# Optimization experiments

Measured on AMD Instinct MI355X. Metric: run time of the kernel, lower is better.

## Reference

```python
import jax, jax.numpy as jnp
import numpy as np
import math


def _bandwidth(d):
    # gz = 2*Gamma((d+1)/2)/Gamma(d/2); use lgamma for numerical stability.
    gz = 2.0 * math.exp(math.lgamma(0.5 * (d + 1)) - math.lgamma(0.5 * d))
    return 1.0 / (2.0 * gz * gz)


def _kernel_mean(xa, xb, gamma):
    # mean over the [Na, Nb] RBF kernel matrix, squared distance via matmul identity
    sq = (jnp.sum(xa * xa, axis=1)[:, None]
          + jnp.sum(xb * xb, axis=1)[None, :]
          - 2.0 * (xa @ xb.T))
    sq = jnp.maximum(sq, 0.0)  # guard tiny negatives from the identity
    return jnp.mean(jnp.exp(-gamma * sq))


def setup_inputs() -> dict:
    key = jax.random.key(0)
    k1, k2 = jax.random.split(key)
    x1 = jax.random.normal(k1, (8192, 128), dtype=jnp.float32)
    x2 = jax.random.normal(k2, (8192, 128), dtype=jnp.float32)
    return {"x1": x1, "x2": x2}


def reference(x1, x2):
    g1 = _bandwidth(x1.shape[1])
    g2 = _bandwidth(x2.shape[1])
    m11 = _kernel_mean(x1, x1, g1)
    m22 = _kernel_mean(x2, x2, g2)
    m12 = _kernel_mean(x1, x2, g1)
    return jnp.sqrt(m11 - 2.0 * m12 + m22)
```

## Files before the change

### kernel.cpp

```cpp
#include <hip/hip_runtime.h>
#include <cmath>

#define D 128
#define BM 128
#define BK 64
#define LOG2E 1.4426950408889634

typedef __attribute__((ext_vector_type(8))) _Float16 f16x8;
typedef __attribute__((ext_vector_type(4))) float f32x4;
typedef __attribute__((ext_vector_type(2))) float f32x2;

__device__ __forceinline__ void async_cp16(const void* g, void* l) {
    __builtin_amdgcn_global_load_lds(
        (__attribute__((address_space(1))) void*)g,
        (__attribute__((address_space(3))) void*)l, 16, 0, 0);
}

__global__ __launch_bounds__(256) void prep_kernel(
    const float* __restrict__ x1, const float* __restrict__ x2,
    _Float16* __restrict__ xh, float* __restrict__ El,
    double* __restrict__ acc, float gl, int N) {
    int tid = threadIdx.x;
    if (blockIdx.x == 0 && tid < 64) acc[tid] = 0.0;
    int r = blockIdx.x * 16 + (tid >> 4);
    if (r >= 2 * N) return;
    int l = tid & 15;
    const float* row = (r < N) ? x1 + (size_t)r * D : x2 + (size_t)(r - N) * D;
    float4 v0 = ((const float4*)row)[l * 2];
    float4 v1 = ((const float4*)row)[l * 2 + 1];
    float v[8] = {v0.x, v0.y, v0.z, v0.w, v1.x, v1.y, v1.z, v1.w};
    float p = 0.f;
    _Float16 h8[8];
#pragma unroll
    for (int j = 0; j < 8; ++j) {
        p = fmaf(v[j], v[j], p);
        h8[j] = (_Float16)v[j];
    }
    *(uint4*)(xh + (size_t)r * D + l * 8) = *(uint4*)h8;
#pragma unroll
    for (int off = 8; off; off >>= 1) p += __shfl_down(p, off, 16);
    if (l == 0) El[r] = gl * p;
}

__global__ __launch_bounds__(256, 4) void mmd_mfma_kernel(
    const _Float16* __restrict__ xh, const float* __restrict__ El,
    double* __restrict__ acc, float c2l, int N) {
    __shared__ float4 smem[2048];

    int t = blockIdx.x;
    int bi = (int)((sqrtf(8.0f * t + 1.0f) - 1.0f) * 0.5f);
    while ((bi + 1) * (bi + 2) / 2 <= t) ++bi;
    while (bi * (bi + 1) / 2 > t) --bi;
    int bj = t - bi * (bi + 1) / 2;

    int half = N / BM;
    float w = (bi == bj) ? 1.0f : 2.0f;
    if ((bi < half) != (bj < half)) w = -2.0f;
    int aBase = bi * BM, bBase = bj * BM;

    int tid = threadIdx.x;
    int lane = tid & 63, wave = tid >> 6;
    int quad = lane >> 4, l16 = lane & 15;
    int wrow = (wave & 1) * 64, wcol = (wave >> 1) * 64;

    const _Float16* gsrc[8];
    float4* ldst[8];
#pragma unroll
    for (int r = 0; r < 2; ++r) {
        int rowBase = r ? bBase : aBase;
#pragma unroll
        for (int i = 0; i < 4; ++i) {
            int slot = i * 256 + tid;
            int row = slot >> 3;
            int kc4 = (slot & 7) ^ (row & 7);
            gsrc[r * 4 + i] = xh + ((size_t)(rowBase + row) * D + kc4 * 8);
            ldst[r * 4 + i] = &smem[r * 1024 + slot];
        }
    }

    f32x4 C[4][4];
#pragma unroll
    for (int i = 0; i < 4; ++i)
#pragma unroll
        for (int j = 0; j < 4; ++j) C[i][j] = {0.f, 0.f, 0.f, 0.f};

    for (int c = 0; c < 2; ++c) {
        if (c) __syncthreads();
        int koff = c * BK;
#pragma unroll
        for (int q = 0; q < 8; ++q) async_cp16(gsrc[q] + koff, ldst[q]);
        __syncthreads();
#pragma unroll
        for (int s = 0; s < 2; ++s) {
            int kc4 = s * 4 + quad;
            f16x8 a[4], b[4];
#pragma unroll
            for (int u = 0; u < 4; ++u) {
                int ar = wrow + u * 16 + l16;
                a[u] = *(const f16x8*)&smem[ar * 8 + (kc4 ^ (ar & 7))];
                int br = wcol + u * 16 + l16;
                b[u] = *(const f16x8*)&smem[1024 + br * 8 + (kc4 ^ (br & 7))];
            }
#pragma unroll
            for (int ti = 0; ti < 4; ++ti)
#pragma unroll
                for (int tj = 0; tj < 4; ++tj)
                    C[ti][tj] = __builtin_amdgcn_mfma_f32_16x16x32_f16(
                        a[ti], b[tj], C[ti][tj], 0, 0, 0);
        }
    }

    int arow0 = aBase + wrow + quad * 4;
    int bcol0 = bBase + wcol + l16;
    float4 ea4[4];
#pragma unroll
    for (int ti = 0; ti < 4; ++ti) ea4[ti] = *(const float4*)&El[arow0 + ti * 16];
    f32x2 cc = {c2l, c2l};
    float lsum = 0.f;
#pragma unroll
    for (int tj = 0; tj < 4; ++tj) {
        float eb = El[bcol0 + tj * 16];
        f32x2 p = {0.f, 0.f};
#pragma unroll
        for (int ti = 0; ti < 4; ++ti) {
            f32x4 d = C[ti][tj];
            f32x2 a01 = cc * f32x2{d.x, d.y} + f32x2{ea4[ti].x, ea4[ti].y};
            f32x2 a23 = cc * f32x2{d.z, d.w} + f32x2{ea4[ti].z, ea4[ti].w};
            f32x2 e, e2;
            e.x = __builtin_amdgcn_exp2f(a01.x);
            e.y = __builtin_amdgcn_exp2f(a01.y);
            e2.x = __builtin_amdgcn_exp2f(a23.x);
            e2.y = __builtin_amdgcn_exp2f(a23.y);
            p += e + e2;
        }
        lsum = fmaf(p.x + p.y, __builtin_amdgcn_exp2f(eb), lsum);
    }
    double ds = (double)lsum * (double)w;
#pragma unroll
    for (int off = 32; off; off >>= 1) ds += __shfl_down(ds, off);
    __syncthreads();
    double* red = (double*)smem;
    if (lane == 0) red[wave] = ds;
    __syncthreads();
    if (tid == 0)
        atomicAdd(&acc[(bi + bj) & 63], red[0] + red[1] + red[2] + red[3]);
}

__global__ __launch_bounds__(64) void mmd_finalize_kernel(
    const double* __restrict__ acc, float* __restrict__ out, int N) {
    int l = threadIdx.x;
    double v = acc[l];
#pragma unroll
    for (int off = 32; off; off >>= 1) v += __shfl_down(v, off);
    if (l == 0) {
        double nn = (double)N * (double)N;
        double s = v / nn;
        out[0] = (float)sqrt(s > 0.0 ? s : 0.0);
    }
}

extern "C" void kernel_launch(void* const* d_in, const int* in_sizes, int n_in,
                              void* d_out, int out_size, void* d_ws, size_t ws_size,
                              hipStream_t stream) {
    const float* x1 = (const float*)d_in[0];
    const float* x2 = (const float*)d_in[1];
    int N = in_sizes[0] / D;

    double* acc = (double*)d_ws;
    float* El = (float*)((char*)d_ws + 8192);
    _Float16* xh = (_Float16*)((char*)d_ws + 73728);

    double lg = lgamma(0.5 * (D + 1)) - lgamma(0.5 * D);
    double gz = 2.0 * exp(lg);
    double gamma = 1.0 / (2.0 * gz * gz);
    float gl = (float)(-gamma * LOG2E);
    float c2l = (float)(2.0 * gamma * LOG2E);

    prep_kernel<<<(2 * N + 15) / 16, 256, 0, stream>>>(x1, x2, xh, El, acc, gl, N);

    int nt2 = 2 * N / BM;
    int nblocks = nt2 * (nt2 + 1) / 2;
    mmd_mfma_kernel<<<nblocks, 256, 0, stream>>>(xh, El, acc, c2l, N);

    mmd_finalize_kernel<<<1, 64, 0, stream>>>(acc, (float*)d_out, N);
}
```

Measured before the change: 109.4 us.

## Load MFMA operands directly from global memory instead of staging through LDS

```diff
diff --git a/kernel.cpp b/kernel.cpp
--- a/kernel.cpp
+++ b/kernel.cpp
@@ -3,18 +3,11 @@
 
 #define D 128
 #define BM 128
-#define BK 64
 #define LOG2E 1.4426950408889634
 
 typedef __attribute__((ext_vector_type(8))) _Float16 f16x8;
 typedef __attribute__((ext_vector_type(4))) float f32x4;
 typedef __attribute__((ext_vector_type(2))) float f32x2;
-
-__device__ __forceinline__ void async_cp16(const void* g, void* l) {
-    __builtin_amdgcn_global_load_lds(
-        (__attribute__((address_space(1))) void*)g,
-        (__attribute__((address_space(3))) void*)l, 16, 0, 0);
-}
 
 __global__ __launch_bounds__(256) void prep_kernel(
     const float* __restrict__ x1, const float* __restrict__ x2,
@@ -45,7 +38,7 @@
 __global__ __launch_bounds__(256, 4) void mmd_mfma_kernel(
     const _Float16* __restrict__ xh, const float* __restrict__ El,
     double* __restrict__ acc, float c2l, int N) {
-    __shared__ float4 smem[2048];
+    __shared__ double red[4];
 
     int t = blockIdx.x;
     int bi = (int)((sqrtf(8.0f * t + 1.0f) - 1.0f) * 0.5f);
@@ -63,19 +56,12 @@
     int quad = lane >> 4, l16 = lane & 15;
     int wrow = (wave & 1) * 64, wcol = (wave >> 1) * 64;
 
-    const _Float16* gsrc[8];
-    float4* ldst[8];
+    const char* xb = (const char*)xh;
+    unsigned offA[4], offB[4];
 #pragma unroll
-    for (int r = 0; r < 2; ++r) {
-        int rowBase = r ? bBase : aBase;
-#pragma unroll
-        for (int i = 0; i < 4; ++i) {
-            int slot = i * 256 + tid;
-            int row = slot >> 3;
-            int kc4 = (slot & 7) ^ (row & 7);
-            gsrc[r * 4 + i] = xh + ((size_t)(rowBase + row) * D + kc4 * 8);
-            ldst[r * 4 + i] = &smem[r * 1024 + slot];
-        }
+    for (int u = 0; u < 4; ++u) {
+        offA[u] = (unsigned)(aBase + wrow + u * 16 + l16) * 256u + (unsigned)quad * 16u;
+        offB[u] = (unsigned)(bBase + wcol + u * 16 + l16) * 256u + (unsigned)quad * 16u;
     }
 
     f32x4 C[4][4];
@@ -84,30 +70,20 @@
 #pragma unroll
         for (int j = 0; j < 4; ++j) C[i][j] = {0.f, 0.f, 0.f, 0.f};
 
-    for (int c = 0; c < 2; ++c) {
-        if (c) __syncthreads();
-        int koff = c * BK;
 #pragma unroll
-        for (int q = 0; q < 8; ++q) async_cp16(gsrc[q] + koff, ldst[q]);
-        __syncthreads();
+    for (int s = 0; s < 4; ++s) {
+        f16x8 a[4], b[4];
 #pragma unroll
-        for (int s = 0; s < 2; ++s) {
-            int kc4 = s * 4 + quad;
-            f16x8 a[4], b[4];
+        for (int u = 0; u < 4; ++u) {
+            a[u] = *(const f16x8*)(xb + offA[u] + s * 64);
+            b[u] = *(const f16x8*)(xb + offB[u] + s * 64);
+        }
 #pragma unroll
-            for (int u = 0; u < 4; ++u) {
-                int ar = wrow + u * 16 + l16;
-                a[u] = *(const f16x8*)&smem[ar * 8 + (kc4 ^ (ar & 7))];
-                int br = wcol + u * 16 + l16;
-                b[u] = *(const f16x8*)&smem[1024 + br * 8 + (kc4 ^ (br & 7))];
-            }
+        for (int ti = 0; ti < 4; ++ti)
 #pragma unroll
-            for (int ti = 0; ti < 4; ++ti)
-#pragma unroll
-                for (int tj = 0; tj < 4; ++tj)
-                    C[ti][tj] = __builtin_amdgcn_mfma_f32_16x16x32_f16(
-                        a[ti], b[tj], C[ti][tj], 0, 0, 0);
-        }
+            for (int tj = 0; tj < 4; ++tj)
+                C[ti][tj] = __builtin_amdgcn_mfma_f32_16x16x32_f16(
+                    a[ti], b[tj], C[ti][tj], 0, 0, 0);
     }
 
     int arow0 = aBase + wrow + quad * 4;
@@ -138,8 +114,6 @@
     double ds = (double)lsum * (double)w;
 #pragma unroll
     for (int off = 32; off; off >>= 1) ds += __shfl_down(ds, off);
-    __syncthreads();
-    double* red = (double*)smem;
     if (lane == 0) red[wave] = ds;
     __syncthreads();
     if (tid == 0)
```

After: 185.8 us. 1.7x slower.
